# Optimization experiments

Hardware: AMD Instinct MI355X
Metric: run time of the kernel (lower is better)

## Reference

```python
import jax, jax.numpy as jnp
import numpy as np

E = 20    # number of residue types (rc.restypes)
NB = 2    # num_blocks per AngleHead
NA = 7    # num_angles
C_S = 384
C_H = 128
BS, L = 8, 2048


def setup_inputs() -> dict:
    key = jax.random.key(0)
    ks = jax.random.split(key, 16)
    sc = 0.02
    return {
        "s": jax.random.normal(ks[0], (BS, L, C_S), dtype=jnp.float32),
        "s_init": jax.random.normal(ks[1], (BS, L, C_S), dtype=jnp.float32),
        "aatype": jax.random.randint(ks[2], (BS, L), 0, E, dtype=jnp.int32),
        # stacked per-residue-type AngleHead params
        "Win": jax.random.normal(ks[3], (E, C_S, C_H), dtype=jnp.float32) * sc,
        "b_in": jax.random.normal(ks[4], (E, C_H), dtype=jnp.float32) * sc,
        "Winit": jax.random.normal(ks[5], (E, C_S, C_H), dtype=jnp.float32) * sc,
        "b_init2": jax.random.normal(ks[6], (E, C_H), dtype=jnp.float32) * sc,
        "Wb1": jax.random.normal(ks[7], (E, NB, C_H, C_H), dtype=jnp.float32) * sc,
        "bb1": jax.random.normal(ks[8], (E, NB, C_H), dtype=jnp.float32) * sc,
        "Wb2": jax.random.normal(ks[9], (E, NB, C_H, C_H), dtype=jnp.float32) * sc,
        "bb2": jax.random.normal(ks[10], (E, NB, C_H), dtype=jnp.float32) * sc,
        "Wout": jax.random.normal(ks[11], (E, C_H, NA * 2), dtype=jnp.float32) * sc,
        "b_out": jax.random.normal(ks[12], (E, NA * 2), dtype=jnp.float32) * sc,
    }


def reference(s, s_init, aatype, Win, b_in, Winit, b_init2, Wb1, bb1, Wb2, bb2, Wout, b_out):
    relu = jax.nn.relu
    bs, seq_len, c_s = s.shape
    N = bs * seq_len
    sf = s.reshape(N, c_s)          # [N, c_s]
    si = s_init.reshape(N, c_s)     # [N, c_s]

    # Dense dispatch: run every token through all E per-type heads, then
    # combine with the one-hot routing mask (math identical to the torch
    # gather/scatter loop over residue types).
    h = jnp.einsum('nd,edh->neh', relu(sf), Win) + b_in            # [N,E,H]
    h = h + jnp.einsum('nd,edh->neh', relu(si), Winit) + b_init2   # [N,E,H]

    for b in range(NB):  # ResidualBlock1d: s + W2 @ relu(W1 @ relu(s))
        a = jnp.einsum('neh,ehk->nek', relu(h), Wb1[:, b]) + bb1[:, b]
        a = jnp.einsum('nek,ekh->neh', relu(a), Wb2[:, b]) + bb2[:, b]
        h = h + a

    out = jnp.einsum('neh,eho->neo', relu(h), Wout) + b_out        # [N,E,2*NA]
    sel = jax.nn.one_hot(aatype.reshape(N), E, dtype=out.dtype)    # [N,E]
    ang = jnp.einsum('neo,ne->no', out, sel).reshape(bs, seq_len, NA, 2)

    # F.normalize(dim=-1): x / max(||x||, eps)
    nrm = jnp.maximum(jnp.linalg.norm(ang, axis=-1, keepdims=True), 1e-12)
    return ang / nrm
```

## Files before the change

### kernel.cpp

```cpp
#include <hip/hip_runtime.h>
#include <math.h>

#define E_TYPES 20
#define NBLK 2
#define NANG 7
#define CS 384
#define CH 128
#define N_TOK (8 * 2048)
#define TOK 32
#define TPB 512
#define PREPB 256
#define MAX_TILES (N_TOK / TOK + E_TYPES)
#define GRID_M 536
#define PADN 2048

#define CNT_OFF 0
#define PERM_OFF 64
#define WT1_OFF (256 * 1024)
#define WT1_SZ  (20 * 8 * 24 * 2048)
#define WTR_OFF (WT1_OFF + WT1_SZ)

typedef __attribute__((ext_vector_type(8))) short bfrag;
typedef __attribute__((ext_vector_type(4))) float f32x4;

__device__ __forceinline__ void split_bf16(float x, unsigned short& h, unsigned short& l) {
    unsigned int u = __float_as_uint(x);
    unsigned int hb = (u + 0x7FFFu + ((u >> 16) & 1u)) & 0xFFFF0000u;
    h = (unsigned short)(hb >> 16);
    float r = x - __uint_as_float(hb);
    unsigned int v = __float_as_uint(r);
    l = (unsigned short)((v + 0x7FFFu + ((v >> 16) & 1u)) >> 16);
}

__global__ __launch_bounds__(PREPB)
void prep_k(const float* __restrict__ Win, const float* __restrict__ Winit,
            const float* __restrict__ Wb1, const float* __restrict__ Wb2,
            const int* __restrict__ aatype, int* __restrict__ wsI,
            unsigned short* __restrict__ wt)
{
    __shared__ unsigned short tp[4][2][32][134];
    __shared__ int lh[E_TYPES], lcur[E_TYPES];
    int bid = blockIdx.x, t = threadIdx.x;

    if (bid < 64) {
        if (t < E_TYPES) { lh[t] = 0; lcur[t] = 0; }
        __syncthreads();
        for (int i = t; i < bid * 256; i += 256) atomicAdd(&lh[aatype[i]], 1);
        __syncthreads();
        int idx = bid * 256 + t;
        int e = aatype[idx];
        int r = lh[e] + atomicAdd(&lcur[e], 1);
        if (r < PADN) wsI[PERM_OFF + e * PADN + r] = idx;
        if (bid == 63) {
            __syncthreads();
            if (t < E_TYPES) wsI[CNT_OFF + t] = lh[t] + lcur[t];
        }
        return;
    }

    int w = t >> 6, lane = t & 63, lane15 = lane & 15, quad = lane >> 4;
    int wid = (bid - 64) * 4 + w;
    const float* srcbase;
    int phase1, e, kt, m4 = 0;
    if (wid < 480) {
        phase1 = 1;
        e = wid / 24; kt = wid % 24;
        srcbase = (kt < 12) ? Win   + ((size_t)e * CS + kt * 32) * CH
                            : Winit + ((size_t)e * CS + (kt - 12) * 32) * CH;
    } else {
        phase1 = 0;
        int rid = wid - 480;
        e = rid >> 4; m4 = (rid >> 2) & 3; kt = rid & 3;
        const float* W = (m4 & 1) ? Wb2 : Wb1;
        srcbase = W + (((size_t)e * NBLK + (m4 >> 1)) * CH + kt * 32) * CH;
    }

    #pragma unroll 4
    for (int i = 0; i < 16; i++) {
        int idx = i * 64 + lane;
        int row = idx >> 5, c4 = idx & 31;
        float4 v = *(const float4*)(srcbase + (size_t)row * CH + c4 * 4);
        ushort4 hv, lv;
        split_bf16(v.x, hv.x, lv.x);
        split_bf16(v.y, hv.y, lv.y);
        split_bf16(v.z, hv.z, lv.z);
        split_bf16(v.w, hv.w, lv.w);
        *(ushort4*)&tp[w][0][row][c4 * 4] = hv;
        *(ushort4*)&tp[w][1][row][c4 * 4] = lv;
    }
    #pragma unroll
    for (int nt = 0; nt < 8; nt++) {
        bfrag hb, lb;
        #pragma unroll
        for (int j = 0; j < 8; j++) {
            hb[j] = (short)tp[w][0][quad * 8 + j][nt * 16 + lane15];
            lb[j] = (short)tp[w][1][quad * 8 + j][nt * 16 + lane15];
        }
        size_t blk = phase1 ? (size_t)((e * 8 + nt) * 24 + kt)
                            : (size_t)((((e * 4 + m4) * 8) + nt) * 4 + kt);
        unsigned short* dst = wt + (phase1 ? WT1_OFF / 2 : WTR_OFF / 2)
                              + blk * 1024 + lane * 8;
        *(bfrag*)dst = hb;
        *(bfrag*)(dst + 512) = lb;
    }
}

#define MFMA(a, b, c) __builtin_amdgcn_mfma_f32_16x16x32_bf16((a), (b), (c), 0, 0, 0)

__global__ __launch_bounds__(TPB)
void angle_main(const float* __restrict__ s, const float* __restrict__ si,
                const float* __restrict__ b_in, const float* __restrict__ b_init2,
                const float* __restrict__ bb1, const float* __restrict__ bb2,
                const float* __restrict__ Wout, const float* __restrict__ b_out,
                const int* __restrict__ wsI, const unsigned short* __restrict__ wt,
                float* __restrict__ out)
{
    __shared__ __align__(16) unsigned char smem_raw[32768];
    typedef unsigned short AfragT[2][2][512][8];
    AfragT& Afrag = *reinterpret_cast<AfragT*>(smem_raw);
    float (*Hf)[130] = reinterpret_cast<float(*)[130]>(smem_raw);
    float (*Of)[16]  = reinterpret_cast<float(*)[16]>(smem_raw + 16640);
    __shared__ int ptok[TOK];
    __shared__ int poffs[E_TYPES + 1];

    int t = threadIdx.x;
    if (t == 0) {
        int off = 0;
        for (int e = 0; e < E_TYPES; e++) {
            poffs[e] = off;
            off += (wsI[CNT_OFF + e] + TOK - 1) & ~(TOK - 1);
        }
        poffs[E_TYPES] = off;
    }
    __syncthreads();

    int bid = blockIdx.x;
    int tile = (bid & 7) * (GRID_M / 8) + (bid >> 3);
    int pos = tile * TOK;
    if (pos >= poffs[E_TYPES]) return;
    int e = 0;
    while (e < E_TYPES - 1 && pos >= poffs[e + 1]) e++;
    int n = wsI[CNT_OFF + e] - (pos - poffs[e]);
    if (n > TOK) n = TOK;
    if (t < TOK)
        ptok[t] = wsI[PERM_OFF + e * PADN + (pos - poffs[e]) + ((t < n) ? t : 0)];

    int w = t >> 6, lane = t & 63, lane15 = lane & 15, quad = lane >> 4;
    int mw = w >> 2;
    int np = w & 3;
    int nc0 = (2 * np) * 16 + lane15, nc1 = nc0 + 16;

    __syncthreads();

    const bfrag* wt1 = (const bfrag*)((const char*)wt + WT1_OFF);
    const bfrag* wtr = (const bfrag*)((const char*)wt + WTR_OFF);

    f32x4 acc[2];
    {
        float bv0 = b_in[e * CH + nc0] + b_init2[e * CH + nc0];
        float bv1 = b_in[e * CH + nc1] + b_init2[e * CH + nc1];
        acc[0] = (f32x4){bv0, bv0, bv0, bv0};
        acc[1] = (f32x4){bv1, bv1, bv1, bv1};
    }

    int stok = t >> 4, sc = t & 15;
    const float* rowp_s  = s  + (size_t)ptok[stok] * CS;
    const float* rowp_si = si + (size_t)ptok[stok] * CS;

    float4 pf[2][2];
    #pragma unroll
    for (int q = 0; q < 2; q++)
        pf[0][q] = *(const float4*)(rowp_s + sc * 4 + 64 * q);

    #pragma unroll
    for (int c = 0; c < 6; c++) {
        int buf = c & 1;
        __syncthreads();
        #pragma unroll
        for (int q = 0; q < 2; q++) {
            float4 v = pf[buf][q];
            ushort4 hv, lv;
            split_bf16(fmaxf(v.x, 0.f), hv.x, lv.x);
            split_bf16(fmaxf(v.y, 0.f), hv.y, lv.y);
            split_bf16(fmaxf(v.z, 0.f), hv.z, lv.z);
            split_bf16(fmaxf(v.w, 0.f), hv.w, lv.w);
            int fi = ((sc >> 1) + 8 * q) * 32 + stok;
            *(ushort4*)&Afrag[buf][0][fi][(sc & 1) * 4] = hv;
            *(ushort4*)&Afrag[buf][1][fi][(sc & 1) * 4] = lv;
        }
        if (c + 1 < 6) {
            const float* rp = ((c + 1) < 3 ? rowp_s : rowp_si) + ((c + 1) % 3) * 128;
            #pragma unroll
            for (int q = 0; q < 2; q++)
                pf[(c + 1) & 1][q] = *(const float4*)(rp + sc * 4 + 64 * q);
        }
        __syncthreads();
        #pragma unroll
        for (int ks = 0; ks < 4; ks++) {
            int kb = c * 4 + ks;
            int fib = (ks * 4 + quad) * 32 + mw * 16;
            bfrag ah = *(const bfrag*)&Afrag[buf][0][fib + lane15][0];
            bfrag al = *(const bfrag*)&Afrag[buf][1][fib + lane15][0];
            size_t b0 = ((size_t)(e * 8 + 2 * np) * 24 + kb) * 128;
            size_t b1 = ((size_t)(e * 8 + 2 * np + 1) * 24 + kb) * 128;
            bfrag bh0 = wt1[b0 + lane], bl0 = wt1[b0 + 64 + lane];
            bfrag bh1 = wt1[b1 + lane], bl1 = wt1[b1 + 64 + lane];
            acc[0] = MFMA(ah, bh0, acc[0]);
            acc[0] = MFMA(ah, bl0, acc[0]);
            acc[0] = MFMA(al, bh0, acc[0]);
            acc[1] = MFMA(ah, bh1, acc[1]);
            acc[1] = MFMA(ah, bl1, acc[1]);
            acc[1] = MFMA(al, bh1, acc[1]);
        }
    }

    f32x4 a2[2];
    #pragma unroll
    for (int b = 0; b < NBLK; b++) {
        #pragma unroll
        for (int stage = 0; stage < 2; stage++) {
            int g = 2 * b + stage;
            __syncthreads();
            #pragma unroll
            for (int nl = 0; nl < 2; nl++) {
                f32x4 v = (stage == 0) ? acc[nl] : a2[nl];
                int nn = (2 * np + nl) * 16 + lane15;
                int fib = ((nn >> 5) * 4 + ((nn >> 3) & 3)) * 32;
                int j = nn & 7;
                #pragma unroll
                for (int r = 0; r < 4; r++) {
                    int m = mw * 16 + quad * 4 + r;
                    unsigned short hh, ll;
                    split_bf16(fmaxf(v[r], 0.f), hh, ll);
                    Afrag[0][0][fib + m][j] = hh;
                    Afrag[0][1][fib + m][j] = ll;
                }
            }
            __syncthreads();

            const float* bias = (stage == 0) ? bb1 : bb2;
            f32x4 an[2];
            {
                float bv0 = bias[(e * NBLK + b) * CH + nc0];
                float bv1 = bias[(e * NBLK + b) * CH + nc1];
                an[0] = (f32x4){bv0, bv0, bv0, bv0};
                an[1] = (f32x4){bv1, bv1, bv1, bv1};
            }
            #pragma unroll
            for (int ks = 0; ks < 4; ks++) {
                int fib = (ks * 4 + quad) * 32 + mw * 16;
                bfrag ah = *(const bfrag*)&Afrag[0][0][fib + lane15][0];
                bfrag al = *(const bfrag*)&Afrag[0][1][fib + lane15][0];
                size_t b0 = ((size_t)((e * 4 + g) * 8 + 2 * np) * 4 + ks) * 128;
                size_t b1 = ((size_t)((e * 4 + g) * 8 + 2 * np + 1) * 4 + ks) * 128;
                bfrag bh0 = wtr[b0 + lane], bl0 = wtr[b0 + 64 + lane];
                bfrag bh1 = wtr[b1 + lane], bl1 = wtr[b1 + 64 + lane];
                an[0] = MFMA(ah, bh0, an[0]);
                an[0] = MFMA(ah, bl0, an[0]);
                an[0] = MFMA(al, bh0, an[0]);
                an[1] = MFMA(ah, bh1, an[1]);
                an[1] = MFMA(ah, bl1, an[1]);
                an[1] = MFMA(al, bh1, an[1]);
            }
            if (stage == 0) {
                a2[0] = an[0]; a2[1] = an[1];
            } else {
                acc[0] += an[0]; acc[1] += an[1];
            }
        }
    }

    __syncthreads();
    #pragma unroll
    for (int nl = 0; nl < 2; nl++) {
        f32x4 v = acc[nl];
        int nn = (2 * np + nl) * 16 + lane15;
        #pragma unroll
        for (int r = 0; r < 4; r++)
            Hf[mw * 16 + quad * 4 + r][nn] = fmaxf(v[r], 0.f);
    }
    __syncthreads();

    const float* WoutE = Wout + (size_t)e * CH * (NANG * 2);
    const float* boutE = b_out + (size_t)e * (NANG * 2);
    for (int idx = t; idx < n * (NANG * 2); idx += TPB) {
        int i = idx / (NANG * 2);
        int o = idx % (NANG * 2);
        float v = boutE[o];
        #pragma unroll 4
        for (int k = 0; k < CH; k++)
            v = fmaf(Hf[i][k], WoutE[(size_t)k * (NANG * 2) + o], v);
        Of[i][o] = v;
    }
    __syncthreads();

    for (int idx = t; idx < n * NANG; idx += TPB) {
        int i = idx / NANG;
        int a = idx % NANG;
        float x = Of[i][2 * a];
        float y = Of[i][2 * a + 1];
        float nr = fmaxf(sqrtf(x * x + y * y), 1e-12f);
        size_t base = (size_t)ptok[i] * (NANG * 2) + 2 * a;
        out[base]     = x / nr;
        out[base + 1] = y / nr;
    }
}

extern "C" void kernel_launch(void* const* d_in, const int* in_sizes, int n_in,
                              void* d_out, int out_size, void* d_ws, size_t ws_size,
                              hipStream_t stream) {
    const float* s       = (const float*)d_in[0];
    const float* s_init  = (const float*)d_in[1];
    const int*   aatype  = (const int*)d_in[2];
    const float* Win     = (const float*)d_in[3];
    const float* b_in    = (const float*)d_in[4];
    const float* Winit   = (const float*)d_in[5];
    const float* b_init2 = (const float*)d_in[6];
    const float* Wb1     = (const float*)d_in[7];
    const float* bb1     = (const float*)d_in[8];
    const float* Wb2     = (const float*)d_in[9];
    const float* bb2     = (const float*)d_in[10];
    const float* Wout    = (const float*)d_in[11];
    const float* b_out   = (const float*)d_in[12];
    int* wsI = (int*)d_ws;
    unsigned short* wt = (unsigned short*)d_ws;
    float* out = (float*)d_out;

    hipLaunchKernelGGL(prep_k, dim3(64 + 200), dim3(PREPB), 0, stream,
                       Win, Winit, Wb1, Wb2, aatype, wsI, wt);
    hipLaunchKernelGGL(angle_main, dim3(GRID_M), dim3(TPB), 0, stream,
                       s, s_init, b_in, b_init2, bb1, bb2, Wout, b_out,
                       wsI, wt, out);
}
```

Before: 174.9 us.

## Restructure main kernel to single-wave 16-token tiles with no barriers

The main kernel now uses one 64-thread wave per block handling 16 tokens and all 128 output channels, in place of 8 waves over 32 tokens. This removes every __syncthreads and uses an XOR-swizzled LDS layout for the A fragments. The weight-prep kernel is split into four times as many smaller wave tasks, so more blocks share the conversion. The trade-off is that each wave now streams the full per-type weight matrix itself, so weight traffic per token roughly doubles and there is less parallelism within a block.

```diff
diff --git a/kernel.cpp b/kernel.cpp
--- a/kernel.cpp
+++ b/kernel.cpp
@@ -7,11 +7,9 @@
 #define CS 384
 #define CH 128
 #define N_TOK (8 * 2048)
-#define TOK 32
-#define TPB 512
+#define TOK 16
 #define PREPB 256
-#define MAX_TILES (N_TOK / TOK + E_TYPES)
-#define GRID_M 536
+#define GRID_M 1080
 #define PADN 2048
 
 #define CNT_OFF 0
@@ -38,7 +36,7 @@
             const int* __restrict__ aatype, int* __restrict__ wsI,
             unsigned short* __restrict__ wt)
 {
-    __shared__ unsigned short tp[4][2][32][134];
+    __shared__ unsigned short tp[4][2][32][34];
     __shared__ int lh[E_TYPES], lcur[E_TYPES];
     int bid = blockIdx.x, t = threadIdx.x;
 
@@ -60,41 +58,42 @@
 
     int w = t >> 6, lane = t & 63, lane15 = lane & 15, quad = lane >> 4;
     int wid = (bid - 64) * 4 + w;
+    if (wid >= 3200) return;
     const float* srcbase;
-    int phase1, e, kt, m4 = 0;
-    if (wid < 480) {
+    int phase1, e, kt, pr, m4 = 0;
+    if (wid < 1920) {
         phase1 = 1;
-        e = wid / 24; kt = wid % 24;
-        srcbase = (kt < 12) ? Win   + ((size_t)e * CS + kt * 32) * CH
-                            : Winit + ((size_t)e * CS + (kt - 12) * 32) * CH;
+        e = wid / 96; int rem = wid % 96; kt = rem >> 2; pr = rem & 3;
+        srcbase = ((kt < 12) ? Win   + ((size_t)e * CS + kt * 32) * CH
+                             : Winit + ((size_t)e * CS + (kt - 12) * 32) * CH) + pr * 32;
     } else {
         phase1 = 0;
-        int rid = wid - 480;
-        e = rid >> 4; m4 = (rid >> 2) & 3; kt = rid & 3;
+        int rid = wid - 1920;
+        e = rid / 64; int rem = rid % 64; m4 = rem >> 4; kt = (rem >> 2) & 3; pr = rem & 3;
         const float* W = (m4 & 1) ? Wb2 : Wb1;
-        srcbase = W + (((size_t)e * NBLK + (m4 >> 1)) * CH + kt * 32) * CH;
-    }
-
-    #pragma unroll 4
-    for (int i = 0; i < 16; i++) {
-        int idx = i * 64 + lane;
-        int row = idx >> 5, c4 = idx & 31;
-        float4 v = *(const float4*)(srcbase + (size_t)row * CH + c4 * 4);
+        srcbase = W + (((size_t)e * NBLK + (m4 >> 1)) * CH + kt * 32) * CH + pr * 32;
+    }
+
+    #pragma unroll
+    for (int i = 0; i < 4; i++) {
+        int row = i * 8 + (lane >> 3), col = (lane & 7) * 4;
+        float4 v = *(const float4*)(srcbase + (size_t)row * CH + col);
         ushort4 hv, lv;
         split_bf16(v.x, hv.x, lv.x);
         split_bf16(v.y, hv.y, lv.y);
         split_bf16(v.z, hv.z, lv.z);
         split_bf16(v.w, hv.w, lv.w);
-        *(ushort4*)&tp[w][0][row][c4 * 4] = hv;
-        *(ushort4*)&tp[w][1][row][c4 * 4] = lv;
-    }
-    #pragma unroll
-    for (int nt = 0; nt < 8; nt++) {
+        *(ushort4*)&tp[w][0][row][col] = hv;
+        *(ushort4*)&tp[w][1][row][col] = lv;
+    }
+    #pragma unroll
+    for (int h = 0; h < 2; h++) {
+        int nt = pr * 2 + h;
         bfrag hb, lb;
         #pragma unroll
         for (int j = 0; j < 8; j++) {
-            hb[j] = (short)tp[w][0][quad * 8 + j][nt * 16 + lane15];
-            lb[j] = (short)tp[w][1][quad * 8 + j][nt * 16 + lane15];
+            hb[j] = (short)tp[w][0][quad * 8 + j][h * 16 + lane15];
+            lb[j] = (short)tp[w][1][quad * 8 + j][h * 16 + lane15];
         }
         size_t blk = phase1 ? (size_t)((e * 8 + nt) * 24 + kt)
                             : (size_t)((((e * 4 + m4) * 8) + nt) * 4 + kt);
@@ -107,7 +106,7 @@
 
 #define MFMA(a, b, c) __builtin_amdgcn_mfma_f32_16x16x32_bf16((a), (b), (c), 0, 0, 0)
 
-__global__ __launch_bounds__(TPB)
+__global__ __launch_bounds__(64)
 void angle_main(const float* __restrict__ s, const float* __restrict__ si,
                 const float* __restrict__ b_in, const float* __restrict__ b_init2,
                 const float* __restrict__ bb1, const float* __restrict__ bb2,
@@ -115,175 +114,168 @@
                 const int* __restrict__ wsI, const unsigned short* __restrict__ wt,
                 float* __restrict__ out)
 {
-    __shared__ __align__(16) unsigned char smem_raw[32768];
-    typedef unsigned short AfragT[2][2][512][8];
-    AfragT& Afrag = *reinterpret_cast<AfragT*>(smem_raw);
-    float (*Hf)[130] = reinterpret_cast<float(*)[130]>(smem_raw);
-    float (*Of)[16]  = reinterpret_cast<float(*)[16]>(smem_raw + 16640);
-    __shared__ int ptok[TOK];
-    __shared__ int poffs[E_TYPES + 1];
-
-    int t = threadIdx.x;
-    if (t == 0) {
-        int off = 0;
-        for (int e = 0; e < E_TYPES; e++) {
-            poffs[e] = off;
-            off += (wsI[CNT_OFF + e] + TOK - 1) & ~(TOK - 1);
-        }
-        poffs[E_TYPES] = off;
-    }
-    __syncthreads();
+    __shared__ __align__(16) unsigned short A[2][2048];
+    __shared__ float Hf[16][132];
+    __shared__ float Of[16][16];
+
+    int lane = threadIdx.x & 63;
+    int lane15 = lane & 15, quad = lane >> 4;
 
     int bid = blockIdx.x;
     int tile = (bid & 7) * (GRID_M / 8) + (bid >> 3);
     int pos = tile * TOK;
-    if (pos >= poffs[E_TYPES]) return;
-    int e = 0;
-    while (e < E_TYPES - 1 && pos >= poffs[e + 1]) e++;
-    int n = wsI[CNT_OFF + e] - (pos - poffs[e]);
+
+    int e = -1, rel = 0, cnt_e = 0, off = 0;
+    #pragma unroll
+    for (int ee = 0; ee < E_TYPES; ee++) {
+        int c = wsI[CNT_OFF + ee];
+        int pad = (c + TOK - 1) & ~(TOK - 1);
+        if (e < 0 && pos < off + pad) { e = ee; rel = pos - off; cnt_e = c; }
+        off += pad;
+    }
+    if (e < 0) return;
+    int n = cnt_e - rel;
     if (n > TOK) n = TOK;
-    if (t < TOK)
-        ptok[t] = wsI[PERM_OFF + e * PADN + (pos - poffs[e]) + ((t < n) ? t : 0)];
-
-    int w = t >> 6, lane = t & 63, lane15 = lane & 15, quad = lane >> 4;
-    int mw = w >> 2;
-    int np = w & 3;
-    int nc0 = (2 * np) * 16 + lane15, nc1 = nc0 + 16;
-
-    __syncthreads();
-
-    const bfrag* wt1 = (const bfrag*)((const char*)wt + WT1_OFF);
-    const bfrag* wtr = (const bfrag*)((const char*)wt + WTR_OFF);
-
-    f32x4 acc[2];
-    {
-        float bv0 = b_in[e * CH + nc0] + b_init2[e * CH + nc0];
-        float bv1 = b_in[e * CH + nc1] + b_init2[e * CH + nc1];
-        acc[0] = (f32x4){bv0, bv0, bv0, bv0};
-        acc[1] = (f32x4){bv1, bv1, bv1, bv1};
-    }
-
-    int stok = t >> 4, sc = t & 15;
-    const float* rowp_s  = s  + (size_t)ptok[stok] * CS;
-    const float* rowp_si = si + (size_t)ptok[stok] * CS;
-
-    float4 pf[2][2];
-    #pragma unroll
-    for (int q = 0; q < 2; q++)
-        pf[0][q] = *(const float4*)(rowp_s + sc * 4 + 64 * q);
-
-    #pragma unroll
-    for (int c = 0; c < 6; c++) {
-        int buf = c & 1;
-        __syncthreads();
-        #pragma unroll
-        for (int q = 0; q < 2; q++) {
-            float4 v = pf[buf][q];
-            ushort4 hv, lv;
-            split_bf16(fmaxf(v.x, 0.f), hv.x, lv.x);
-            split_bf16(fmaxf(v.y, 0.f), hv.y, lv.y);
-            split_bf16(fmaxf(v.z, 0.f), hv.z, lv.z);
-            split_bf16(fmaxf(v.w, 0.f), hv.w, lv.w);
-            int fi = ((sc >> 1) + 8 * q) * 32 + stok;
-            *(ushort4*)&Afrag[buf][0][fi][(sc & 1) * 4] = hv;
-            *(ushort4*)&Afrag[buf][1][fi][(sc & 1) * 4] = lv;
-        }
-        if (c + 1 < 6) {
-            const float* rp = ((c + 1) < 3 ? rowp_s : rowp_si) + ((c + 1) % 3) * 128;
-            #pragma unroll
-            for (int q = 0; q < 2; q++)
-                pf[(c + 1) & 1][q] = *(const float4*)(rp + sc * 4 + 64 * q);
-        }
-        __syncthreads();
-        #pragma unroll
-        for (int ks = 0; ks < 4; ks++) {
-            int kb = c * 4 + ks;
-            int fib = (ks * 4 + quad) * 32 + mw * 16;
-            bfrag ah = *(const bfrag*)&Afrag[buf][0][fib + lane15][0];
-            bfrag al = *(const bfrag*)&Afrag[buf][1][fib + lane15][0];
-            size_t b0 = ((size_t)(e * 8 + 2 * np) * 24 + kb) * 128;
-            size_t b1 = ((size_t)(e * 8 + 2 * np + 1) * 24 + kb) * 128;
-            bfrag bh0 = wt1[b0 + lane], bl0 = wt1[b0 + 64 + lane];
-            bfrag bh1 = wt1[b1 + lane], bl1 = wt1[b1 + 64 + lane];
-            acc[0] = MFMA(ah, bh0, acc[0]);
-            acc[0] = MFMA(ah, bl0, acc[0]);
-            acc[0] = MFMA(al, bh0, acc[0]);
-            acc[1] = MFMA(ah, bh1, acc[1]);
-            acc[1] = MFMA(ah, bl1, acc[1]);
-            acc[1] = MFMA(al, bh1, acc[1]);
-        }
-    }
-
-    f32x4 a2[2];
-    #pragma unroll
-    for (int b = 0; b < NBLK; b++) {
-        #pragma unroll
-        for (int stage = 0; stage < 2; stage++) {
-            int g = 2 * b + stage;
-            __syncthreads();
-            #pragma unroll
-            for (int nl = 0; nl < 2; nl++) {
-                f32x4 v = (stage == 0) ? acc[nl] : a2[nl];
-                int nn = (2 * np + nl) * 16 + lane15;
-                int fib = ((nn >> 5) * 4 + ((nn >> 3) & 3)) * 32;
-                int j = nn & 7;
-                #pragma unroll
-                for (int r = 0; r < 4; r++) {
-                    int m = mw * 16 + quad * 4 + r;
-                    unsigned short hh, ll;
-                    split_bf16(fmaxf(v[r], 0.f), hh, ll);
-                    Afrag[0][0][fib + m][j] = hh;
-                    Afrag[0][1][fib + m][j] = ll;
-                }
-            }
-            __syncthreads();
-
-            const float* bias = (stage == 0) ? bb1 : bb2;
-            f32x4 an[2];
-            {
-                float bv0 = bias[(e * NBLK + b) * CH + nc0];
-                float bv1 = bias[(e * NBLK + b) * CH + nc1];
-                an[0] = (f32x4){bv0, bv0, bv0, bv0};
-                an[1] = (f32x4){bv1, bv1, bv1, bv1};
-            }
-            #pragma unroll
-            for (int ks = 0; ks < 4; ks++) {
-                int fib = (ks * 4 + quad) * 32 + mw * 16;
-                bfrag ah = *(const bfrag*)&Afrag[0][0][fib + lane15][0];
-                bfrag al = *(const bfrag*)&Afrag[0][1][fib + lane15][0];
-                size_t b0 = ((size_t)((e * 4 + g) * 8 + 2 * np) * 4 + ks) * 128;
-                size_t b1 = ((size_t)((e * 4 + g) * 8 + 2 * np + 1) * 4 + ks) * 128;
-                bfrag bh0 = wtr[b0 + lane], bl0 = wtr[b0 + 64 + lane];
-                bfrag bh1 = wtr[b1 + lane], bl1 = wtr[b1 + 64 + lane];
-                an[0] = MFMA(ah, bh0, an[0]);
-                an[0] = MFMA(ah, bl0, an[0]);
-                an[0] = MFMA(al, bh0, an[0]);
-                an[1] = MFMA(ah, bh1, an[1]);
-                an[1] = MFMA(ah, bl1, an[1]);
-                an[1] = MFMA(al, bh1, an[1]);
-            }
-            if (stage == 0) {
-                a2[0] = an[0]; a2[1] = an[1];
-            } else {
-                acc[0] += an[0]; acc[1] += an[1];
-            }
-        }
-    }
-
-    __syncthreads();
-    #pragma unroll
-    for (int nl = 0; nl < 2; nl++) {
-        f32x4 v = acc[nl];
-        int nn = (2 * np + nl) * 16 + lane15;
+
+    int m = lane >> 2, g = lane & 3;
+    int trow = (m < n) ? m : (n - 1);
+    int tok = wsI[PERM_OFF + e * PADN + rel + trow];
+    const float* rowp_s  = s  + (size_t)tok * CS;
+    const float* rowp_si = si + (size_t)tok * CS;
+
+    const char* wt1b = (const char*)wt + WT1_OFF;
+    const char* wtrb = (const char*)wt + WTR_OFF;
+
+    f32x4 acc[8];
+    #pragma unroll
+    for (int nt = 0; nt < 8; nt++) {
+        int ch = nt * 16 + lane15;
+        float bv = b_in[e * CH + ch] + b_init2[e * CH + ch];
+        acc[nt] = (f32x4){bv, bv, bv, bv};
+    }
+
+    float4 pf[4];
+    #pragma unroll
+    for (int q = 0; q < 4; q++)
+        pf[q] = *(const float4*)(rowp_s + g * 16 + q * 4);
+
+    int ks0 = g >> 1, qd0 = 2 * (g & 1);
+
+    for (int c = 0; c < 12; c++) {
+        #pragma unroll
+        for (int hf = 0; hf < 2; hf++) {
+            float4 va = pf[hf * 2], vb = pf[hf * 2 + 1];
+            ushort4 h0, l0, h1, l1;
+            split_bf16(fmaxf(va.x, 0.f), h0.x, l0.x);
+            split_bf16(fmaxf(va.y, 0.f), h0.y, l0.y);
+            split_bf16(fmaxf(va.z, 0.f), h0.z, l0.z);
+            split_bf16(fmaxf(va.w, 0.f), h0.w, l0.w);
+            split_bf16(fmaxf(vb.x, 0.f), h1.x, l1.x);
+            split_bf16(fmaxf(vb.y, 0.f), h1.y, l1.y);
+            split_bf16(fmaxf(vb.z, 0.f), h1.z, l1.z);
+            split_bf16(fmaxf(vb.w, 0.f), h1.w, l1.w);
+            int bse = ks0 * 4 + qd0 + hf;
+            int fi8 = (bse * 16 + (m ^ bse)) * 8;
+            *(ushort4*)&A[0][fi8]     = h0;
+            *(ushort4*)&A[0][fi8 + 4] = h1;
+            *(ushort4*)&A[1][fi8]     = l0;
+            *(ushort4*)&A[1][fi8 + 4] = l1;
+        }
+        if (c + 1 < 12) {
+            const float* rp = ((c + 1) < 6 ? rowp_s : rowp_si) + ((c + 1) % 6) * 64 + g * 16;
+            #pragma unroll
+            for (int q = 0; q < 4; q++)
+                pf[q] = *(const float4*)(rp + q * 4);
+        }
+        #pragma unroll
+        for (int ks = 0; ks < 2; ks++) {
+            int kb = c * 2 + ks;
+            int bse = ks * 4 + quad;
+            int fi8 = (bse * 16 + (lane15 ^ bse)) * 8;
+            bfrag ah = *(const bfrag*)&A[0][fi8];
+            bfrag al = *(const bfrag*)&A[1][fi8];
+            bfrag bh[8], bl[8];
+            #pragma unroll
+            for (int nt = 0; nt < 8; nt++) {
+                const char* p = wt1b + (size_t)((e * 8 + nt) * 24 + kb) * 2048 + lane * 16;
+                bh[nt] = *(const bfrag*)p;
+                bl[nt] = *(const bfrag*)(p + 1024);
+            }
+            #pragma unroll
+            for (int nt = 0; nt < 8; nt++) {
+                acc[nt] = MFMA(ah, bh[nt], acc[nt]);
+                acc[nt] = MFMA(ah, bl[nt], acc[nt]);
+                acc[nt] = MFMA(al, bh[nt], acc[nt]);
+            }
+        }
+    }
+
+    f32x4 a2[8];
+    #pragma unroll
+    for (int gg = 0; gg < 4; gg++) {
+        int b = gg >> 1, second = gg & 1;
+        #pragma unroll
+        for (int nt = 0; nt < 8; nt++) {
+            int bse = (nt >> 1) * 4 + (nt & 1) * 2 + (lane15 >> 3);
+            int j = lane15 & 7;
+            f32x4 v = second ? a2[nt] : acc[nt];
+            #pragma unroll
+            for (int r = 0; r < 4; r++) {
+                int mr = quad * 4 + r;
+                int fi8 = (bse * 16 + (mr ^ bse)) * 8 + j;
+                unsigned short hh, ll;
+                split_bf16(fmaxf(v[r], 0.f), hh, ll);
+                A[0][fi8] = hh;
+                A[1][fi8] = ll;
+            }
+        }
+        const float* bias = second ? bb2 : bb1;
+        f32x4 an[8];
+        #pragma unroll
+        for (int nt = 0; nt < 8; nt++) {
+            float bv = bias[(e * NBLK + b) * CH + nt * 16 + lane15];
+            an[nt] = (f32x4){bv, bv, bv, bv};
+        }
+        #pragma unroll
+        for (int kb = 0; kb < 4; kb++) {
+            int bse = kb * 4 + quad;
+            int fi8 = (bse * 16 + (lane15 ^ bse)) * 8;
+            bfrag ah = *(const bfrag*)&A[0][fi8];
+            bfrag al = *(const bfrag*)&A[1][fi8];
+            bfrag bh[8], bl[8];
+            #pragma unroll
+            for (int nt = 0; nt < 8; nt++) {
+                const char* p = wtrb + (size_t)(((e * 4 + gg) * 8 + nt) * 4 + kb) * 2048 + lane * 16;
+                bh[nt] = *(const bfrag*)p;
+                bl[nt] = *(const bfrag*)(p + 1024);
+            }
+            #pragma unroll
+            for (int nt = 0; nt < 8; nt++) {
+                an[nt] = MFMA(ah, bh[nt], an[nt]);
+                an[nt] = MFMA(ah, bl[nt], an[nt]);
+                an[nt] = MFMA(al, bh[nt], an[nt]);
+            }
+        }
+        if (!second) {
+            #pragma unroll
+            for (int nt = 0; nt < 8; nt++) a2[nt] = an[nt];
+        } else {
+            #pragma unroll
+            for (int nt = 0; nt < 8; nt++) acc[nt] += an[nt];
+        }
+    }
+
+    #pragma unroll
+    for (int nt = 0; nt < 8; nt++) {
+        f32x4 v = acc[nt];
         #pragma unroll
         for (int r = 0; r < 4; r++)
-            Hf[mw * 16 + quad * 4 + r][nn] = fmaxf(v[r], 0.f);
-    }
-    __syncthreads();
+            Hf[quad * 4 + r][nt * 16 + lane15] = fmaxf(v[r], 0.f);
+    }
 
     const float* WoutE = Wout + (size_t)e * CH * (NANG * 2);
     const float* boutE = b_out + (size_t)e * (NANG * 2);
-    for (int idx = t; idx < n * (NANG * 2); idx += TPB) {
+    for (int idx = lane; idx < n * (NANG * 2); idx += 64) {
         int i = idx / (NANG * 2);
         int o = idx % (NANG * 2);
         float v = boutE[o];
@@ -292,15 +284,15 @@
             v = fmaf(Hf[i][k], WoutE[(size_t)k * (NANG * 2) + o], v);
         Of[i][o] = v;
     }
-    __syncthreads();
-
-    for (int idx = t; idx < n * NANG; idx += TPB) {
+
+    for (int idx = lane; idx < n * NANG; idx += 64) {
         int i = idx / NANG;
         int a = idx % NANG;
         float x = Of[i][2 * a];
         float y = Of[i][2 * a + 1];
         float nr = fmaxf(sqrtf(x * x + y * y), 1e-12f);
-        size_t base = (size_t)ptok[i] * (NANG * 2) + 2 * a;
+        int ti = wsI[PERM_OFF + e * PADN + rel + i];
+        size_t base = (size_t)ti * (NANG * 2) + 2 * a;
         out[base]     = x / nr;
         out[base + 1] = y / nr;
     }
@@ -326,9 +318,9 @@
     unsigned short* wt = (unsigned short*)d_ws;
     float* out = (float*)d_out;
 
-    hipLaunchKernelGGL(prep_k, dim3(64 + 200), dim3(PREPB), 0, stream,
+    hipLaunchKernelGGL(prep_k, dim3(64 + 800), dim3(PREPB), 0, stream,
                        Win, Winit, Wb1, Wb2, aatype, wsI, wt);
-    hipLaunchKernelGGL(angle_main, dim3(GRID_M), dim3(TPB), 0, stream,
+    hipLaunchKernelGGL(angle_main, dim3(GRID_M), dim3(64), 0, stream,
                        s, s_init, b_in, b_init2, bb1, bb2, Wout, b_out,
                        wsI, wt, out);
 }
```

New measurement: 202.8 us. +16.0%, slower.
